# Performance work log

Measured on AMD Instinct MI355X. Metric: run time of the kernel, lower is better.

Reference implementation:

```python
import math
import jax, jax.numpy as jnp
import numpy as np

B, T, E, H = 8, 2048, 512, 8
NQ_H, NL = 4, 2          # qubits per attention head, circuit layers
NQ_F, FFN = 8, 2048      # FFN qubits, ffn_dim

# ---- batched state-vector quantum simulation -------------------------------
# state shape: [N, 2, 2, ..., 2] (one axis of size 2 per qubit; wire q = axis q+1)

def apply_ry(state, q, theta):
    """RY(theta) on wire q. theta: scalar or [N] (per-batch angle)."""
    th = jnp.asarray(theta) * 0.5
    c, s = jnp.cos(th), jnp.sin(th)
    if th.ndim == 1:
        shp = (-1,) + (1,) * (state.ndim - 2)
        c, s = c.reshape(shp), s.reshape(shp)
    s0 = jax.lax.index_in_dim(state, 0, axis=q + 1, keepdims=False)
    s1 = jax.lax.index_in_dim(state, 1, axis=q + 1, keepdims=False)
    return jnp.stack([c * s0 - s * s1, s * s0 + c * s1], axis=q + 1)

def apply_cnot(state, ctrl, tgt):
    c0 = jax.lax.index_in_dim(state, 0, axis=ctrl + 1, keepdims=True)
    c1 = jax.lax.index_in_dim(state, 1, axis=ctrl + 1, keepdims=True)
    c1 = jnp.flip(c1, axis=tgt + 1)  # X on target when control = 1
    return jnp.concatenate([c0, c1], axis=ctrl + 1)

def run_circuit(x, params):
    """x: [N, n] data angles. params: [L, n] (shared) or [N, L, n] (per-element).
    Circuit: L x (RY(params) layer + CNOT chain + ring CNOT), then RY(x), then <Z_q>.
    Returns [N, n] PauliZ expectations."""
    N, n = x.shape
    L = params.shape[-2]
    state = jnp.zeros((N, 2 ** n), x.dtype).at[:, 0].set(1.0).reshape((N,) + (2,) * n)
    for l in range(L):
        for q in range(n):
            theta = params[:, l, q] if params.ndim == 3 else params[l, q]
            state = apply_ry(state, q, theta)
        for q in range(n - 1):
            state = apply_cnot(state, q, q + 1)
        state = apply_cnot(state, n - 1, 0)
    for q in range(n):
        state = apply_ry(state, q, x[:, q])
    probs = (state ** 2).reshape(N, 2 ** n)
    bits = (jnp.arange(2 ** n)[:, None] >> (n - 1 - jnp.arange(n))) & 1  # wire 0 = MSB
    return probs @ (1 - 2 * bits).astype(x.dtype)  # [N, n]

def layer_norm(x, g, b, eps=1e-5):
    m = x.mean(-1, keepdims=True)
    v = ((x - m) ** 2).mean(-1, keepdims=True)
    return (x - m) / jnp.sqrt(v + eps) * g + b

def setup_inputs() -> dict:
    key = jax.random.key(0)
    ks = jax.random.split(key, 9)
    def lin(k, o, i):
        return jax.random.normal(k, (o, i), jnp.float32) / np.sqrt(i).astype(np.float32)
    return {
        "x": jax.random.normal(ks[0], (B, T, E), jnp.float32),
        "wq": lin(ks[1], E, E), "wk": lin(ks[2], E, E),
        "wv": lin(ks[3], E, E), "wo": lin(ks[4], E, E),
        "head_params": jax.random.normal(ks[5], (H, NL, NQ_H), jnp.float32),
        "ffn_params": jax.random.normal(ks[6], (2, NQ_F), jnp.float32),
        "w1": lin(ks[7], FFN, NQ_F), "w2": lin(ks[8], E, FFN),
        "g1": jnp.ones((E,), jnp.float32), "b1": jnp.zeros((E,), jnp.float32),
        "g2": jnp.ones((E,), jnp.float32), "b2": jnp.zeros((E,), jnp.float32),
    }

def reference(x, wq, wk, wv, wo, head_params, ffn_params, w1, w2, g1, b1, g2, b2):
    Bb, Tt, Ee = x.shape
    hd = Ee // H
    BT = Bb * Tt
    # ---- quantum multi-head attention (dropout = eval/identity) ----
    q = x @ wq.T; k = x @ wk.T; v = x @ wv.T
    scores = jnp.einsum('bte,bse->bts', q, k) / math.sqrt(Ee)  # NOTE: scale by sqrt(E)
    attn = jax.nn.softmax(scores, axis=-1)
    out = jnp.einsum('bts,bse->bte', attn, v)                  # [B,T,E]
    oh = out.reshape(Bb, Tt, H, hd)
    # fold heads into the batch dim; per-head params broadcast per element
    xh = oh[..., :NQ_H].transpose(2, 0, 1, 3).reshape(H * BT, NQ_H)
    ph = jnp.broadcast_to(head_params[:, None], (H, BT, NL, NQ_H)).reshape(H * BT, NL, NQ_H)
    qout = run_circuit(xh, ph)                                  # [H*BT, NQ_H]
    qout = jnp.pad(qout, ((0, 0), (0, hd - NQ_H)))              # zero-pad to head_dim
    qout = qout.reshape(H, Bb, Tt, hd).transpose(1, 2, 0, 3).reshape(Bb, Tt, Ee)
    attn_out = qout @ wo.T
    x1 = layer_norm(x + attn_out, g1, b1)
    # ---- quantum FFN (only ffn_params[0] used, as in source) ----
    xf = x1.reshape(BT, Ee)[:, :NQ_F]
    f = run_circuit(xf, ffn_params[:1]).reshape(Bb, Tt, NQ_F)
    f = jax.nn.relu(f @ w1.T) @ w2.T
    return layer_norm(x1 + f, g2, b2)
```

## Files before the change

kernel.cpp:

```cpp
#include <hip/hip_runtime.h>
#include <hip/hip_bf16.h>
#include <math.h>


#define B_   8
#define T_   2048
#define E_   512

typedef __attribute__((ext_vector_type(8))) short bf16x8;
typedef __attribute__((ext_vector_type(4))) short bf16x4;
typedef __attribute__((ext_vector_type(4))) float f32x4;

#define GLL16(g, l) __builtin_amdgcn_global_load_lds((const __attribute__((address_space(1))) void*)(g), (__attribute__((address_space(3))) void*)(l), 16, 0, 0)

__device__ inline unsigned short f2bf(float f){
  union { float f; unsigned u; } v; v.f = f;
  unsigned r = v.u + 0x7fff + ((v.u >> 16) & 1);
  return (unsigned short)(r >> 16);
}

__global__ __launch_bounds__(256) void k0_setup(const float* __restrict__ hp,
                         const float* __restrict__ fp,
                         const float* __restrict__ wo, float* __restrict__ cAB,
                         unsigned short* __restrict__ wo32b) {
  int t = threadIdx.x, bi = blockIdx.x;
  if (bi > 0) {
    int gid = (bi-1)*256 + t;
    int e = gid >> 3, c4 = gid & 7;
    float4 v = *(const float4*)(wo + (size_t)e*512 + c4*64);
    unsigned short h[4] = { f2bf(v.x), f2bf(v.y), f2bf(v.z), f2bf(v.w) };
    *(unsigned long long*)(wo32b + (size_t)e*32 + c4*4) = *(unsigned long long*)h;
    return;
  }
  __shared__ float fst[256], tmp[256], ra[256], rb[256];
  fst[t] = (t == 0) ? 1.f : 0.f;
  __syncthreads();
  #pragma unroll
  for (int q = 0; q < 8; ++q) {
    int str = 1 << (7-q);
    float th = 0.5f * fp[q];
    float c = cosf(th), s = sinf(th);
    float self = fst[t], part = fst[t ^ str];
    float nv = (t & str) ? (c*self + s*part) : (c*self - s*part);
    __syncthreads();
    tmp[t] = nv;
    __syncthreads();
    fst[t] = tmp[t];
    __syncthreads();
  }
  #pragma unroll
  for (int g = 0; g < 8; ++g) {
    int ctrl = (g < 7) ? g : 7, tgt = (g < 7) ? g+1 : 0;
    int cs = 1 << (7-ctrl), tsr = 1 << (7-tgt);
    float nv = fst[(t & cs) ? (t ^ tsr) : t];
    __syncthreads();
    fst[t] = nv;
    __syncthreads();
  }
  #pragma unroll
  for (int q = 0; q < 8; ++q) {
    int str = 1 << (7-q);
    float a = fst[t]*fst[t] * ((t & str) ? -1.f : 1.f);
    float b = fst[t]*fst[t ^ str];
    ra[t] = a; rb[t] = b;
    __syncthreads();
    for (int off = 128; off > 0; off >>= 1){
      if (t < off){ ra[t] += ra[t+off]; rb[t] += rb[t+off]; }
      __syncthreads();
    }
    if (t == 0){ cAB[64+q] = ra[0]; cAB[72+q] = rb[0]; }
    __syncthreads();
  }
  if (t < 8) {
    float st[16];
    #pragma unroll
    for (int i=0;i<16;i++) st[i]=0.f;
    st[0]=1.f;
    for (int l=0;l<2;l++){
      for (int q=0;q<4;q++){
        float th = 0.5f*hp[t*8 + l*4 + q];
        float c = cosf(th), s = sinf(th);
        int str = 1<<(3-q);
        for (int i=0;i<16;i++) if (!(i & str)) {
          float s0=st[i], s1=st[i|str];
          st[i]     = c*s0 - s*s1;
          st[i|str] = s*s0 + c*s1;
        }
      }
      for (int q=0;q<4;q++){
        int ctrl = (q<3)? q : 3, tgt = (q<3)? q+1 : 0;
        int cs = 1<<(3-ctrl), tsr = 1<<(3-tgt);
        for (int i=0;i<16;i++) if ((i&cs) && !(i&tsr)) {
          float tt = st[i]; st[i]=st[i|tsr]; st[i|tsr]=tt;
        }
      }
    }
    for (int q=0;q<4;q++){
      int str = 1<<(3-q);
      float A=0.f, Bv=0.f;
      for (int i=0;i<16;i++){
        A  += st[i]*st[i] * ((i&str)? -1.f : 1.f);
        Bv += st[i]*st[i^str];
      }
      cAB[t*4+q]    = A;
      cAB[32+t*4+q] = Bv;
    }
  }
}

__global__ __launch_bounds__(256) void kc_cast(const float* __restrict__ x,
                     const float* __restrict__ wq, const float* __restrict__ wk,
                     const float* __restrict__ w2, const float* __restrict__ wv,
                     unsigned short* __restrict__ xb, unsigned short* __restrict__ wqkb,
                     unsigned short* __restrict__ w2b, unsigned short* __restrict__ wv32b){
  int bi = blockIdx.x;
  if (bi < 4096) {
    int i = bi*256 + threadIdx.x;
    const float4* p = (const float4*)x + (size_t)i*2;
    float4 a = p[0], b = p[1];
    union { unsigned short h[8]; uint4 u; } o;
    o.h[0]=f2bf(a.x); o.h[1]=f2bf(a.y); o.h[2]=f2bf(a.z); o.h[3]=f2bf(a.w);
    o.h[4]=f2bf(b.x); o.h[5]=f2bf(b.y); o.h[6]=f2bf(b.z); o.h[7]=f2bf(b.w);
    ((uint4*)xb)[i] = o.u;
    return;
  }
  int i = (bi-4096)*256 + threadIdx.x;
  const float* src; unsigned short* dst; float s = 1.f;
  if (i < 65536){
    int row = i >> 6, c8 = (i & 63)*8;
    if (row < 512){ src = wq + (size_t)row*512 + c8; s = 0.044194173824159216f; }
    else          { src = wk + (size_t)(row-512)*512 + c8; }
    dst = wqkb + (size_t)row*512 + c8;
  } else if (i < 196608){
    int j = i - 65536;
    src = w2 + (size_t)j*8; dst = w2b + (size_t)j*8;
  } else {
    int j = i - 196608;
    int r = j >> 6, c8 = (j & 63)*8;
    src = wv + (size_t)((r>>2)*64 + (r&3))*512 + c8;
    dst = wv32b + (size_t)r*512 + c8;
  }
  float4 a = *(const float4*)src, b = *(const float4*)(src+4);
  union { unsigned short h[8]; uint4 u; } o;
  o.h[0]=f2bf(a.x*s); o.h[1]=f2bf(a.y*s); o.h[2]=f2bf(a.z*s); o.h[3]=f2bf(a.w*s);
  o.h[4]=f2bf(b.x*s); o.h[5]=f2bf(b.y*s); o.h[6]=f2bf(b.z*s); o.h[7]=f2bf(b.w*s);
  *(uint4*)dst = o.u;
}

template<int K, int LDC, bool OUTBF, int GX, int GM>
__global__ __launch_bounds__(256,2) void gemm_bt(
    const unsigned short* __restrict__ A, const unsigned short* __restrict__ Bw,
    void* __restrict__ C, int m_base){
  __shared__ __align__(16) char sm[16384];
  char* As = sm; char* Bs = sm + 8192;
  int t = threadIdx.x, w = t>>6, l = t&63;
  int lr = l&15, quad = l>>4;
  int lin = blockIdx.x;
  int n0 = ((lin >> 3) % GX) * 128;
  int m0 = ((lin & 7) * (GM/8) + lin / (8*GX)) * 128;
  int wr = (w>>1)*64, wc = (w&1)*64;
  f32x4 acc[4][4] = {};
  for (int k0 = 0; k0 < K; k0 += 32){
    __syncthreads();
    #pragma unroll
    for (int c = 0; c < 2; ++c){
      int ch = c*256 + t, row = ch>>2, sw = ch&3, lc = sw ^ ((row>>1)&3);
      GLL16(A  + (size_t)(m0+row)*K + k0 + lc*8, As + c*4096 + w*1024);
      GLL16(Bw + (size_t)(n0+row)*K + k0 + lc*8, Bs + c*4096 + w*1024);
    }
    __syncthreads();
    bf16x8 af[4], bg[4];
    #pragma unroll
    for (int i=0;i<4;++i){
      int ra = wr + i*16 + lr;
      af[i] = *(const bf16x8*)(As + ra*64 + (quad ^ ((ra>>1)&3))*16);
      int rb = wc + i*16 + lr;
      bg[i] = *(const bf16x8*)(Bs + rb*64 + (quad ^ ((rb>>1)&3))*16);
    }
    #pragma unroll
    for (int i=0;i<4;++i)
      #pragma unroll
      for (int j=0;j<4;++j)
        acc[i][j] = __builtin_amdgcn_mfma_f32_16x16x32_bf16(af[i], bg[j], acc[i][j], 0,0,0);
  }
  #pragma unroll
  for (int i=0;i<4;++i)
    #pragma unroll
    for (int j=0;j<4;++j)
      #pragma unroll
      for (int r=0;r<4;++r){
        size_t row = (size_t)(m_base + m0 + wr + i*16 + quad*4 + r);
        int col = n0 + wc + j*16 + lr;
        if constexpr (OUTBF) ((unsigned short*)C)[row*LDC + col] = f2bf(acc[i][j][r]);
        else                 ((float*)C)[row*LDC + col] = acc[i][j][r];
      }
}

__global__ __launch_bounds__(256) void k1_v32m(const unsigned short* __restrict__ xb,
    const unsigned short* __restrict__ wv32b, unsigned short* __restrict__ v32t){
  __shared__ __align__(16) char sm1[98304];
  char* Xs = sm1; char* Ws = sm1 + 65536;
  int t = threadIdx.x, w = t>>6, l = t&63, lr = l&15, quad = l>>4;
  int m0 = blockIdx.x * 64;
  #pragma unroll
  for (int i=0;i<16;++i){
    int p = i*256 + t, ks = p>>8, c2 = p&255, row = c2>>2, swp = c2&3;
    int lc = swp ^ ((row>>1)&3);
    GLL16(xb + (size_t)(m0+row)*512 + ks*32 + lc*8, Xs + (p>>6)*1024);
  }
  #pragma unroll
  for (int i=0;i<8;++i){
    int p = i*256 + t, ks = p>>7, c2 = p&127, row = c2>>2, swp = c2&3;
    int lc = swp ^ ((row>>1)&3);
    GLL16(wv32b + (size_t)row*512 + ks*32 + lc*8, Ws + (p>>6)*1024);
  }
  __syncthreads();
  f32x4 acc[2] = {};
  #pragma unroll
  for (int ks=0; ks<16; ++ks){
    int xrow = w*16 + lr;
    bf16x8 bq = *(const bf16x8*)(Xs + ks*4096 + xrow*64 + (quad ^ ((xrow>>1)&3))*16);
    #pragma unroll
    for (int ni=0; ni<2; ++ni){
      int wrow = ni*16 + lr;
      bf16x8 af = *(const bf16x8*)(Ws + ks*2048 + wrow*64 + (quad ^ ((wrow>>1)&3))*16);
      acc[ni] = __builtin_amdgcn_mfma_f32_16x16x32_bf16(af, bq, acc[ni], 0,0,0);
    }
  }
  int bb = m0 >> 11, sbase = (m0 & 2047) + w*16 + lr;
  #pragma unroll
  for (int ni=0; ni<2; ++ni)
    #pragma unroll
    for (int r=0; r<4; ++r){
      int c = ni*16 + quad*4 + r;
      v32t[((size_t)(bb*32 + c))*2048 + sbase] = f2bf(acc[ni][r]);
    }
}

__global__ __launch_bounds__(256,1) void k2_attn(
    const unsigned short* __restrict__ qkb, const unsigned short* __restrict__ v32t,
    float* __restrict__ Opart, float* __restrict__ mlb){
  __shared__ __align__(16) char sm[57856];
  char* Qc  = sm;
  char* Ks  = sm + 8192;
  char* Vts = sm + 40960;
  float* OtL = (float*)sm;
  float* mL  = (float*)(sm + 36864);
  float* lL  = (float*)(sm + 37888);

  int t = threadIdx.x, w = t>>6, l = t&63;
  int lr = l & 15, quad = l >> 4;
  int lin = blockIdx.x;
  int b = lin & 7;
  int m0 = ((lin >> 3) & 31) * 64;
  int half = lin >> 8;
  size_t bT = (size_t)b*2048;
  const char* qbase = (const char*)qkb + (bT + m0)*2048;
  const char* vbase = (const char*)v32t + (size_t)b*32*4096;

  f32x4 Ot[2][4] = {};
  float mold[4] = {-1e30f,-1e30f,-1e30f,-1e30f};
  float lsum[4] = {0.f,0.f,0.f,0.f};

  for (int step = half*4; step < half*4 + 4; ++step){
    int s0 = step*256;
    const char* kbase = (const char*)qkb + (bT + s0)*2048 + 1024;
    __syncthreads();
    {
      int j = t>>3, seg = t&7;
      const uint4* vs = (const uint4*)(vbase + (size_t)j*4096 + (s0 + seg*32)*2);
      uint4* vd = (uint4*)(Vts + j*528 + seg*64);
      vd[0]=vs[0]; vd[1]=vs[1]; vd[2]=vs[2]; vd[3]=vs[3];
    }
    f32x4 acc[4][4] = {};
    for (int ec = 0; ec < 8; ++ec){
      __syncthreads();
      { int row = t>>2, sw = t&3, lc = sw ^ ((row>>1)&3);
        GLL16(qbase + (size_t)row*2048 + ec*128 +      lc*16, Qc +        w*1024);
        GLL16(qbase + (size_t)row*2048 + ec*128 + 64 + lc*16, Qc + 4096 + w*1024);
      }
      #pragma unroll
      for (int rd = 0; rd < 4; ++rd){
        int ch = rd*256 + t, row = ch>>2, sw = ch&3, lc = sw ^ ((row>>1)&3);
        GLL16(kbase + (size_t)row*2048 + ec*128 +      lc*16, Ks +         rd*4096 + w*1024);
        GLL16(kbase + (size_t)row*2048 + ec*128 + 64 + lc*16, Ks + 16384 + rd*4096 + w*1024);
      }
      __syncthreads();
      #pragma unroll
      for (int kk = 0; kk < 2; ++kk){
        bf16x8 af[4], bq[4];
        #pragma unroll
        for (int si = 0; si < 4; ++si){
          int row = w*64 + si*16 + lr;
          af[si] = *(const bf16x8*)(Ks + kk*16384 + row*64 + (quad ^ ((row>>1)&3))*16);
        }
        #pragma unroll
        for (int qj = 0; qj < 4; ++qj){
          int row = qj*16 + lr;
          bq[qj] = *(const bf16x8*)(Qc + kk*4096 + row*64 + (quad ^ ((row>>1)&3))*16);
        }
        #pragma unroll
        for (int si = 0; si < 4; ++si)
          #pragma unroll
          for (int qj = 0; qj < 4; ++qj)
            acc[si][qj] = __builtin_amdgcn_mfma_f32_16x16x32_bf16(af[si], bq[qj], acc[si][qj], 0,0,0);
      }
    }
    bf16x4 aV[2][4];
    #pragma unroll
    for (int vt=0; vt<2; ++vt)
      #pragma unroll
      for (int si=0; si<4; ++si)
        aV[vt][si] = *(const bf16x4*)(Vts + (vt*16+lr)*528 + (w*64 + si*16 + quad*4)*2);
    #pragma unroll
    for (int qj=0; qj<4; ++qj){
      float mt = -1e30f;
      #pragma unroll
      for (int si=0; si<4; ++si)
        #pragma unroll
        for (int r=0;r<4;++r) mt = fmaxf(mt, acc[si][qj][r]);
      mt = fmaxf(mt, __shfl_xor(mt, 16));
      mt = fmaxf(mt, __shfl_xor(mt, 32));
      float mn = fmaxf(mold[qj], mt);
      float al = __expf(mold[qj] - mn);
      mold[qj] = mn;
      float rs = 0.f;
      #pragma unroll
      for (int si=0; si<4; ++si)
        #pragma unroll
        for (int r=0;r<4;++r){
          float p = __expf(acc[si][qj][r] - mn);
          acc[si][qj][r] = p; rs += p;
        }
      rs += __shfl_xor(rs, 16); rs += __shfl_xor(rs, 32);
      lsum[qj] = lsum[qj]*al + rs;
      Ot[0][qj] *= al; Ot[1][qj] *= al;
      #pragma unroll
      for (int si=0; si<4; ++si){
        bf16x4 pb;
        pb[0]=(short)f2bf(acc[si][qj][0]); pb[1]=(short)f2bf(acc[si][qj][1]);
        pb[2]=(short)f2bf(acc[si][qj][2]); pb[3]=(short)f2bf(acc[si][qj][3]);
        Ot[0][qj] = __builtin_amdgcn_mfma_f32_16x16x16bf16_1k(aV[0][si], pb, Ot[0][qj], 0,0,0);
        Ot[1][qj] = __builtin_amdgcn_mfma_f32_16x16x16bf16_1k(aV[1][si], pb, Ot[1][qj], 0,0,0);
      }
    }
  }
  __syncthreads();
  #pragma unroll
  for (int qj=0; qj<4; ++qj){
    if (quad == 0){ mL[w*64 + qj*16 + lr] = mold[qj]; lL[w*64 + qj*16 + lr] = lsum[qj]; }
    *(f32x4*)(OtL + (size_t)(w*64 + qj*16 + lr)*36 + quad*4)      = Ot[0][qj];
    *(f32x4*)(OtL + (size_t)(w*64 + qj*16 + lr)*36 + 16 + quad*4) = Ot[1][qj];
  }
  __syncthreads();
  {
    int qr = t>>2, vg = (t&3)*8;
    float M = -1e30f;
    #pragma unroll
    for (int w4=0; w4<4; ++w4) M = fmaxf(M, mL[w4*64+qr]);
    float L = 0.f; float o[8] = {};
    #pragma unroll
    for (int w4=0; w4<4; ++w4){
      float a = __expf(mL[w4*64+qr] - M);
      L += a * lL[w4*64+qr];
      const float* Op = OtL + (size_t)(w4*64+qr)*36 + vg;
      #pragma unroll
      for (int j=0;j<8;++j) o[j] += a*Op[j];
    }
    size_t tok = bT + m0 + qr;
    float* od = Opart + ((size_t)half*16384 + tok)*32 + vg;
    *(float4*)od     = make_float4(o[0],o[1],o[2],o[3]);
    *(float4*)(od+4) = make_float4(o[4],o[5],o[6],o[7]);
    if ((t&3) == 0){
      mlb[((size_t)half*16384 + tok)*2]     = M;
      mlb[((size_t)half*16384 + tok)*2 + 1] = L;
    }
  }
}

__global__ __launch_bounds__(256) void k2_merge(const float* __restrict__ Opart,
    const float* __restrict__ mlb, const float* __restrict__ cAB,
    unsigned short* __restrict__ q32b){
  int g = blockIdx.x*256 + threadIdx.x;
  int tok = g >> 2, vg = (g & 3) * 8;
  float m0v = mlb[(size_t)tok*2],           l0 = mlb[(size_t)tok*2 + 1];
  float m1v = mlb[(size_t)(16384+tok)*2],   l1 = mlb[(size_t)(16384+tok)*2 + 1];
  float M = fmaxf(m0v, m1v);
  float a0 = __expf(m0v - M), a1 = __expf(m1v - M);
  float inv = 1.f / (a0*l0 + a1*l1);
  const float* O0 = Opart + (size_t)tok*32 + vg;
  const float* O1 = Opart + (size_t)(16384+tok)*32 + vg;
  union { unsigned short h[8]; uint4 u; } res;
  #pragma unroll
  for (int j=0;j<8;++j){
    float ov = (a0*O0[j] + a1*O1[j]) * inv;
    int cc = vg + j;
    res.h[j] = f2bf(cosf(ov)*cAB[cc] - sinf(ov)*cAB[32+cc]);
  }
  *(uint4*)(q32b + (size_t)tok*32 + vg) = res.u;
}

__global__ __launch_bounds__(256) void k3_proj_ln(const float* __restrict__ x,
    const unsigned short* __restrict__ q32b, const unsigned short* __restrict__ wo32b,
    const float* __restrict__ g1, const float* __restrict__ b1,
    const float* __restrict__ cAB, float* __restrict__ x1, float* __restrict__ fbuf) {
  __shared__ __align__(16) char sm3[36224];
  char* Ws = sm3;
  char* Qs = sm3 + 32768;
  float* red1 = (float*)(sm3 + 34816);
  float* red2 = (float*)(sm3 + 35328);
  float* mm   = (float*)(sm3 + 35840);
  float* rr   = (float*)(sm3 + 35968);
  int t = threadIdx.x, w = t>>6, l = t&63, lr = l&15, quad = l>>4;
  int tok0 = blockIdx.x * 32;
  #pragma unroll
  for (int i=0;i<8;++i){
    int g = t + i*256, row = g>>2, ch = g&3;
    uint4 v = ((const uint4*)wo32b)[g];
    *(uint4*)(Ws + row*64 + (ch ^ ((row>>1)&3))*16) = v;
  }
  if (t < 128){
    int row = t>>2, ch = t&3;
    uint4 v = ((const uint4*)(q32b + (size_t)tok0*32))[t];
    *(uint4*)(Qs + row*64 + (ch ^ ((row>>1)&3))*16) = v;
  }
  __syncthreads();
  bf16x8 af[2], bf[8];
  #pragma unroll
  for (int i=0;i<2;++i){
    int m = i*16 + lr;
    af[i] = *(const bf16x8*)(Qs + m*64 + (quad ^ ((m>>1)&3))*16);
  }
  #pragma unroll
  for (int j=0;j<8;++j){
    int n = w*128 + j*16 + lr;
    bf[j] = *(const bf16x8*)(Ws + n*64 + (quad ^ ((n>>1)&3))*16);
  }
  f32x4 acc[2][8];
  #pragma unroll
  for (int i=0;i<2;++i)
    #pragma unroll
    for (int j=0;j<8;++j){
      f32x4 z = {0.f,0.f,0.f,0.f};
      acc[i][j] = __builtin_amdgcn_mfma_f32_16x16x32_bf16(af[i], bf[j], z, 0,0,0);
    }
  float s1[2][4] = {}, s2[2][4] = {};
  #pragma unroll
  for (int i=0;i<2;++i)
    #pragma unroll
    for (int r=0;r<4;++r){
      int m = i*16 + quad*4 + r;
      const float* xrow = x + (size_t)(tok0+m)*512 + w*128 + lr;
      #pragma unroll
      for (int j=0;j<8;++j){
        float v = acc[i][j][r] + xrow[j*16];
        acc[i][j][r] = v;
        s1[i][r] += v; s2[i][r] += v*v;
      }
    }
  #pragma unroll
  for (int off=1; off<16; off<<=1){
    #pragma unroll
    for (int i=0;i<2;++i)
      #pragma unroll
      for (int r=0;r<4;++r){
        s1[i][r] += __shfl_xor(s1[i][r], off);
        s2[i][r] += __shfl_xor(s2[i][r], off);
      }
  }
  if (lr == 0){
    #pragma unroll
    for (int i=0;i<2;++i)
      #pragma unroll
      for (int r=0;r<4;++r){
        int m = i*16 + quad*4 + r;
        red1[w*32 + m] = s1[i][r];
        red2[w*32 + m] = s2[i][r];
      }
  }
  __syncthreads();
  if (t < 32){
    float a = red1[t] + red1[32+t] + red1[64+t] + red1[96+t];
    float bb = red2[t] + red2[32+t] + red2[64+t] + red2[96+t];
    float mean = a * (1.f/512.f);
    float var  = bb * (1.f/512.f) - mean*mean;
    mm[t] = mean; rr[t] = rsqrtf(var + 1e-5f);
  }
  __syncthreads();
  float g1v[8], b1v[8];
  #pragma unroll
  for (int j=0;j<8;++j){
    int n = w*128 + j*16 + lr;
    g1v[j] = g1[n]; b1v[j] = b1[n];
  }
  #pragma unroll
  for (int i=0;i<2;++i)
    #pragma unroll
    for (int r=0;r<4;++r){
      int m = i*16 + quad*4 + r;
      float mean = mm[m], rstd = rr[m];
      float* orow = x1 + (size_t)(tok0+m)*512 + w*128 + lr;
      #pragma unroll
      for (int j=0;j<8;++j){
        float nv = (acc[i][j][r]-mean)*rstd*g1v[j] + b1v[j];
        orow[j*16] = nv;
        if (w == 0 && j == 0 && lr < 8)
          fbuf[(size_t)(tok0+m)*8 + lr] = cosf(nv)*cAB[64+lr] - sinf(nv)*cAB[72+lr];
      }
    }
}

__global__ __launch_bounds__(256) void k4a4(const float* __restrict__ fbuf,
    const float* __restrict__ w1, unsigned short* __restrict__ Hb, int row0){
  __shared__ float w1s[16384];
  int t = threadIdx.x;
  #pragma unroll
  for (int i=0;i<16;++i){
    int p = i*256 + t;
    *(float4*)(w1s + (size_t)p*4) = *(const float4*)(w1 + (size_t)p*4);
  }
  __syncthreads();
  float wv[8][8];
  #pragma unroll
  for (int i=0;i<16;++i){
    float4 v = *(const float4*)(w1s + t*64 + i*4);
    wv[i>>1][(i&1)*4+0]=v.x; wv[i>>1][(i&1)*4+1]=v.y;
    wv[i>>1][(i&1)*4+2]=v.z; wv[i>>1][(i&1)*4+3]=v.w;
  }
  int tokL = blockIdx.x * 32;
  #pragma unroll 2
  for (int u=0;u<32;++u){
    const float4* fp4 = (const float4*)(fbuf + (size_t)(row0 + tokL + u)*8);
    float4 fa = fp4[0], fb = fp4[1];
    union { unsigned short h[8]; uint4 q; } o;
    #pragma unroll
    for (int j=0;j<8;++j){
      float s = fa.x*wv[j][0] + fa.y*wv[j][1] + fa.z*wv[j][2] + fa.w*wv[j][3]
              + fb.x*wv[j][4] + fb.y*wv[j][5] + fb.z*wv[j][6] + fb.w*wv[j][7];
      o.h[j] = f2bf(fmaxf(s, 0.f));
    }
    *(uint4*)(Hb + (size_t)(tokL + u)*2048 + t*8) = o.q;
  }
}

__global__ __launch_bounds__(256) void k5_ln2(const float* __restrict__ x1,
    const float* __restrict__ g2, const float* __restrict__ b2,
    float* __restrict__ out) {
  int tok = blockIdx.x, t = threadIdx.x;
  __shared__ float rs1[4], rs2[4], mv[2];
  float vals[2], ssum=0.f, ssq=0.f;
  #pragma unroll
  for (int u=0;u<2;u++){
    int e = t + u*256;
    float s = x1[(size_t)tok*512 + e] + out[(size_t)tok*512 + e];
    vals[u]=s; ssum+=s; ssq+=s*s;
  }
  #pragma unroll
  for (int off=32; off>0; off>>=1){ ssum += __shfl_down(ssum,off); ssq += __shfl_down(ssq,off); }
  int wid = t >> 6;
  if ((t & 63) == 0){ rs1[wid]=ssum; rs2[wid]=ssq; }
  __syncthreads();
  if (t == 0){
    float a = rs1[0]+rs1[1]+rs1[2]+rs1[3];
    float b = rs2[0]+rs2[1]+rs2[2]+rs2[3];
    float mean = a * (1.f/512.f);
    float var  = b * (1.f/512.f) - mean*mean;
    mv[0]=mean; mv[1]=rsqrtf(var + 1e-5f);
  }
  __syncthreads();
  float mean=mv[0], rstd=mv[1];
  #pragma unroll
  for (int u=0;u<2;u++){
    int e = t + u*256;
    out[(size_t)tok*512 + e] = (vals[u]-mean)*rstd*g2[e] + b2[e];
  }
}

extern "C" void kernel_launch(void* const* d_in, const int* in_sizes, int n_in,
                              void* d_out, int out_size, void* d_ws, size_t ws_size,
                              hipStream_t stream) {
  const float* x  = (const float*)d_in[0];
  const float* wq = (const float*)d_in[1];
  const float* wk = (const float*)d_in[2];
  const float* wv = (const float*)d_in[3];
  const float* wo = (const float*)d_in[4];
  const float* hp = (const float*)d_in[5];
  const float* fp = (const float*)d_in[6];
  const float* w1 = (const float*)d_in[7];
  const float* w2 = (const float*)d_in[8];
  const float* g1 = (const float*)d_in[9];
  const float* b1 = (const float*)d_in[10];
  const float* g2 = (const float*)d_in[11];
  const float* b2 = (const float*)d_in[12];
  float* out = (float*)d_out;
  float* ws  = (float*)d_ws;

  unsigned short* qkb  = (unsigned short*)(ws);
  float*          x1   = ws + 8388608;
  unsigned short* xb   = (unsigned short*)(ws + 16777216);
  unsigned short* wqkb = (unsigned short*)(ws + 20971520);
  unsigned short* w2b  = (unsigned short*)(ws + 21233664);
  unsigned short* v32t = (unsigned short*)(ws + 21757952);
  unsigned short* q32b = (unsigned short*)(ws + 22020096);
  float*          fbuf = ws + 22544384;
  unsigned short* wo32b= (unsigned short*)(ws + 22675456);
  float*          cAB  = ws + 22691840;
  float*          Opart= ws + 22691968;
  float*          mlb  = ws + 23740544;
  unsigned short* wv32b= (unsigned short*)(ws + 23806080);
  unsigned short* Hb   = (unsigned short*)(ws);

  k0_setup<<<17, 256, 0, stream>>>(hp, fp, wo, cAB, wo32b);
  kc_cast<<<4872, 256, 0, stream>>>(x, wq, wk, w2, wv, xb, wqkb, w2b, wv32b);
  gemm_bt<512,1024,true,8,128><<<1024, 256, 0, stream>>>(xb, wqkb, qkb, 0);
  k1_v32m<<<256, 256, 0, stream>>>(xb, wv32b, v32t);
  k2_attn<<<512, 256, 0, stream>>>(qkb, v32t, Opart, mlb);
  k2_merge<<<256, 256, 0, stream>>>(Opart, mlb, cAB, q32b);
  k3_proj_ln<<<512, 256, 0, stream>>>(x, q32b, wo32b, g1, b1, cAB, x1, fbuf);
  k4a4<<<256, 256, 0, stream>>>(fbuf, w1, Hb, 0);
  gemm_bt<2048,512,false,4,64><<<256, 256, 0, stream>>>(Hb, w2b, out, 0);
  k4a4<<<256, 256, 0, stream>>>(fbuf, w1, Hb, 8192);
  gemm_bt<2048,512,false,4,64><<<256, 256, 0, stream>>>(Hb, w2b, out, 8192);
  k5_ln2<<<16384, 256, 0, stream>>>(x1, g2, b2, out);
}
```

Before: 384.6 us.

## Widen attention query tile to 128 rows and split keys four ways

The attention kernel now processes 128 query rows per block instead of 64, doubling reuse of each staged K tile. Each block covers 512 keys instead of 1024, so the key range is split into four partials. The merge kernel is extended to combine four partial softmax states, and the Opart buffer moves into the no-longer-needed xb region. It also raises launch bounds to two blocks per CU and wraps the MFMA bursts in s_setprio. The costs are more LDS per block and more accumulator registers, plus extra partial traffic and a heavier merge step.

```diff
diff --git a/kernel.cpp b/kernel.cpp
--- a/kernel.cpp
+++ b/kernel.cpp
@@ -237,33 +237,34 @@
     }
 }
 
-__global__ __launch_bounds__(256,1) void k2_attn(
+__global__ __launch_bounds__(256,2) void k2_attn(
     const unsigned short* __restrict__ qkb, const unsigned short* __restrict__ v32t,
     float* __restrict__ Opart, float* __restrict__ mlb){
-  __shared__ __align__(16) char sm[57856];
+  __shared__ __align__(16) char sm[77824];
   char* Qc  = sm;
-  char* Ks  = sm + 8192;
-  char* Vts = sm + 40960;
+  char* Ks  = sm + 16384;
+  char* Vts = sm + 49152;
   float* OtL = (float*)sm;
-  float* mL  = (float*)(sm + 36864);
-  float* lL  = (float*)(sm + 37888);
+  float* mL  = (float*)(sm + 73728);
+  float* lL  = (float*)(sm + 75776);
 
   int t = threadIdx.x, w = t>>6, l = t&63;
   int lr = l & 15, quad = l >> 4;
   int lin = blockIdx.x;
   int b = lin & 7;
-  int m0 = ((lin >> 3) & 31) * 64;
-  int half = lin >> 8;
+  int m0 = ((lin >> 3) & 15) * 128;
+  int half = lin >> 7;
   size_t bT = (size_t)b*2048;
   const char* qbase = (const char*)qkb + (bT + m0)*2048;
   const char* vbase = (const char*)v32t + (size_t)b*32*4096;
 
-  f32x4 Ot[2][4] = {};
-  float mold[4] = {-1e30f,-1e30f,-1e30f,-1e30f};
-  float lsum[4] = {0.f,0.f,0.f,0.f};
-
-  for (int step = half*4; step < half*4 + 4; ++step){
-    int s0 = step*256;
+  f32x4 Ot[2][8] = {};
+  float mold[8], lsum[8];
+  #pragma unroll
+  for (int qj=0;qj<8;++qj){ mold[qj] = -1e30f; lsum[qj] = 0.f; }
+
+  for (int st = 0; st < 2; ++st){
+    int s0 = (half*2 + st)*256;
     const char* kbase = (const char*)qkb + (bT + s0)*2048 + 1024;
     __syncthreads();
     {
@@ -272,12 +273,15 @@
       uint4* vd = (uint4*)(Vts + j*528 + seg*64);
       vd[0]=vs[0]; vd[1]=vs[1]; vd[2]=vs[2]; vd[3]=vs[3];
     }
-    f32x4 acc[4][4] = {};
+    f32x4 acc[4][8] = {};
     for (int ec = 0; ec < 8; ++ec){
       __syncthreads();
-      { int row = t>>2, sw = t&3, lc = sw ^ ((row>>1)&3);
-        GLL16(qbase + (size_t)row*2048 + ec*128 +      lc*16, Qc +        w*1024);
-        GLL16(qbase + (size_t)row*2048 + ec*128 + 64 + lc*16, Qc + 4096 + w*1024);
+      #pragma unroll
+      for (int u = 0; u < 4; ++u){
+        int kk = u>>1, c = u&1;
+        int ch = c*256 + t, row = ch>>2, sw = ch&3, lc = sw ^ ((row>>1)&3);
+        GLL16(qbase + (size_t)row*2048 + ec*128 + kk*64 + lc*16,
+              Qc + kk*8192 + c*4096 + w*1024);
       }
       #pragma unroll
       for (int rd = 0; rd < 4; ++rd){
@@ -288,22 +292,28 @@
       __syncthreads();
       #pragma unroll
       for (int kk = 0; kk < 2; ++kk){
-        bf16x8 af[4], bq[4];
+        bf16x8 af[4];
         #pragma unroll
         for (int si = 0; si < 4; ++si){
           int row = w*64 + si*16 + lr;
           af[si] = *(const bf16x8*)(Ks + kk*16384 + row*64 + (quad ^ ((row>>1)&3))*16);
         }
         #pragma unroll
-        for (int qj = 0; qj < 4; ++qj){
-          int row = qj*16 + lr;
-          bq[qj] = *(const bf16x8*)(Qc + kk*4096 + row*64 + (quad ^ ((row>>1)&3))*16);
+        for (int qh = 0; qh < 2; ++qh){
+          bf16x8 bq[4];
+          #pragma unroll
+          for (int jj = 0; jj < 4; ++jj){
+            int row = (qh*4+jj)*16 + lr;
+            bq[jj] = *(const bf16x8*)(Qc + kk*8192 + row*64 + (quad ^ ((row>>1)&3))*16);
+          }
+          __builtin_amdgcn_s_setprio(1);
+          #pragma unroll
+          for (int si = 0; si < 4; ++si)
+            #pragma unroll
+            for (int jj = 0; jj < 4; ++jj)
+              acc[si][qh*4+jj] = __builtin_amdgcn_mfma_f32_16x16x32_bf16(af[si], bq[jj], acc[si][qh*4+jj], 0,0,0);
+          __builtin_amdgcn_s_setprio(0);
         }
-        #pragma unroll
-        for (int si = 0; si < 4; ++si)
-          #pragma unroll
-          for (int qj = 0; qj < 4; ++qj)
-            acc[si][qj] = __builtin_amdgcn_mfma_f32_16x16x32_bf16(af[si], bq[qj], acc[si][qj], 0,0,0);
       }
     }
     bf16x4 aV[2][4];
@@ -313,7 +323,7 @@
       for (int si=0; si<4; ++si)
         aV[vt][si] = *(const bf16x4*)(Vts + (vt*16+lr)*528 + (w*64 + si*16 + quad*4)*2);
     #pragma unroll
-    for (int qj=0; qj<4; ++qj){
+    for (int qj=0; qj<8; ++qj){
       float mt = -1e30f;
       #pragma unroll
       for (int si=0; si<4; ++si)
@@ -347,23 +357,24 @@
   }
   __syncthreads();
   #pragma unroll
-  for (int qj=0; qj<4; ++qj){
-    if (quad == 0){ mL[w*64 + qj*16 + lr] = mold[qj]; lL[w*64 + qj*16 + lr] = lsum[qj]; }
-    *(f32x4*)(OtL + (size_t)(w*64 + qj*16 + lr)*36 + quad*4)      = Ot[0][qj];
-    *(f32x4*)(OtL + (size_t)(w*64 + qj*16 + lr)*36 + 16 + quad*4) = Ot[1][qj];
-  }
-  __syncthreads();
-  {
-    int qr = t>>2, vg = (t&3)*8;
+  for (int qj=0; qj<8; ++qj){
+    if (quad == 0){ mL[w*128 + qj*16 + lr] = mold[qj]; lL[w*128 + qj*16 + lr] = lsum[qj]; }
+    *(f32x4*)(OtL + (size_t)(w*128 + qj*16 + lr)*36 + quad*4)      = Ot[0][qj];
+    *(f32x4*)(OtL + (size_t)(w*128 + qj*16 + lr)*36 + 16 + quad*4) = Ot[1][qj];
+  }
+  __syncthreads();
+  #pragma unroll
+  for (int u=0; u<2; ++u){
+    int qr = u*64 + (t>>2), vg = (t&3)*8;
     float M = -1e30f;
     #pragma unroll
-    for (int w4=0; w4<4; ++w4) M = fmaxf(M, mL[w4*64+qr]);
+    for (int w4=0; w4<4; ++w4) M = fmaxf(M, mL[w4*128+qr]);
     float L = 0.f; float o[8] = {};
     #pragma unroll
     for (int w4=0; w4<4; ++w4){
-      float a = __expf(mL[w4*64+qr] - M);
-      L += a * lL[w4*64+qr];
-      const float* Op = OtL + (size_t)(w4*64+qr)*36 + vg;
+      float a = __expf(mL[w4*128+qr] - M);
+      L += a * lL[w4*128+qr];
+      const float* Op = OtL + (size_t)(w4*128+qr)*36 + vg;
       #pragma unroll
       for (int j=0;j<8;++j) o[j] += a*Op[j];
     }
@@ -383,17 +394,28 @@
     unsigned short* __restrict__ q32b){
   int g = blockIdx.x*256 + threadIdx.x;
   int tok = g >> 2, vg = (g & 3) * 8;
-  float m0v = mlb[(size_t)tok*2],           l0 = mlb[(size_t)tok*2 + 1];
-  float m1v = mlb[(size_t)(16384+tok)*2],   l1 = mlb[(size_t)(16384+tok)*2 + 1];
-  float M = fmaxf(m0v, m1v);
-  float a0 = __expf(m0v - M), a1 = __expf(m1v - M);
-  float inv = 1.f / (a0*l0 + a1*l1);
-  const float* O0 = Opart + (size_t)tok*32 + vg;
-  const float* O1 = Opart + (size_t)(16384+tok)*32 + vg;
+  float m[4], lv[4];
+  #pragma unroll
+  for (int h=0;h<4;++h){
+    m[h]  = mlb[((size_t)h*16384 + tok)*2];
+    lv[h] = mlb[((size_t)h*16384 + tok)*2 + 1];
+  }
+  float M = fmaxf(fmaxf(m[0],m[1]), fmaxf(m[2],m[3]));
+  float a[4], L = 0.f;
+  #pragma unroll
+  for (int h=0;h<4;++h){ a[h] = __expf(m[h]-M); L += a[h]*lv[h]; }
+  float inv = 1.f / L;
+  float o[8] = {};
+  #pragma unroll
+  for (int h=0;h<4;++h){
+    const float* O = Opart + ((size_t)h*16384 + tok)*32 + vg;
+    #pragma unroll
+    for (int j=0;j<8;++j) o[j] += a[h]*O[j];
+  }
   union { unsigned short h[8]; uint4 u; } res;
   #pragma unroll
   for (int j=0;j<8;++j){
-    float ov = (a0*O0[j] + a1*O1[j]) * inv;
+    float ov = o[j] * inv;
     int cc = vg + j;
     res.h[j] = f2bf(cosf(ov)*cAB[cc] - sinf(ov)*cAB[32+cc]);
   }
@@ -605,9 +627,9 @@
   float*          fbuf = ws + 22544384;
   unsigned short* wo32b= (unsigned short*)(ws + 22675456);
   float*          cAB  = ws + 22691840;
-  float*          Opart= ws + 22691968;
-  float*          mlb  = ws + 23740544;
+  float*          mlb  = ws + 22691968;
   unsigned short* wv32b= (unsigned short*)(ws + 23806080);
+  float*          Opart= ws + 16777216;
   unsigned short* Hb   = (unsigned short*)(ws);
 
   k0_setup<<<17, 256, 0, stream>>>(hp, fp, wo, cAB, wo32b);
```

New measurement: 378.3 us. No clear change (-1.6%).
